# Kernel tuning notes

Measured on AMD Instinct MI355X. Metric: run time of the kernel, lower is better.

Reference implementation:

```python
import jax, jax.numpy as jnp
import numpy as np

B, L, D, T = 2, 2048, 1536, 2
INITRANGE = 0.1

def setup_inputs() -> dict:
    key = jax.random.key(0)
    k1, k2 = jax.random.split(key)
    hidden_states = jax.random.normal(k1, (B, L, D), dtype=jnp.float32)
    # decoder: Linear(2*D, T) with uniform(-0.1, 0.1) weight, zero bias
    W = jax.random.uniform(k2, (T, 2 * D), dtype=jnp.float32, minval=-INITRANGE, maxval=INITRANGE)
    b = jnp.zeros((T,), dtype=jnp.float32)
    return {"hidden_states": hidden_states, "W": W, "b": b}

def reference(hidden_states, W, b):
    # Faithful fused version of:
    #   prod = h[:,:,None,:] * h[:,None,:,:]; diff = h[:,:,None,:] - h[:,None,:,:]
    #   logits = cat(prod, diff, -1) @ W.T + b
    # Split W into the product half and the difference half.
    d = hidden_states.shape[-1]
    Wp, Wd = W[:, :d], W[:, d:]                      # [T, D] each
    # prod term: sum_d h[b,i,d] * h[b,j,d] * Wp[t,d]
    hw = jnp.einsum('bid,td->btid', hidden_states, Wp)          # [B,T,L,D]
    prod_logits = jnp.einsum('btid,bjd->bijt', hw, hidden_states)  # [B,L,L,T]
    # diff term: (h[b,i]-h[b,j]) @ Wd.T = (h@Wd.T)[b,i] - (h@Wd.T)[b,j]
    hd = jnp.einsum('bid,td->bit', hidden_states, Wd)           # [B,L,T]
    diff_logits = hd[:, :, None, :] - hd[:, None, :, :]         # [B,L,L,T]
    logits = prod_logits + diff_logits + b
    # symmetrize over the (i, j) pair axes
    logits = (logits + jnp.transpose(logits, (0, 2, 1, 3))) * 0.5
    return logits
```

## Files before the change

kernel.cpp:

```cpp
#include <hip/hip_runtime.h>
#include <hip/hip_bf16.h>
#include <stdint.h>

#define B_ 2
#define L_ 2048
#define D_ 1536

typedef __attribute__((ext_vector_type(4))) float  f32x4;
typedef __attribute__((ext_vector_type(8))) __bf16 bf16x8;

__device__ __forceinline__ unsigned short f2bf(float f) {
  unsigned int u = __float_as_uint(f);
  u += 0x7fffu + ((u >> 16) & 1u);
  return (unsigned short)(u >> 16);
}

__global__ __launch_bounds__(256) void conv_kernel(
    const float* __restrict__ hs, const float* __restrict__ W,
    unsigned short* __restrict__ X, unsigned short* __restrict__ P) {
  const int idx  = blockIdx.x * 256 + threadIdx.x;
  const int base = idx * 4;
  const int d    = base % D_;
  const float4 h  = *(const float4*)(hs + base);
  const float4 w0 = *(const float4*)(W + d);
  const float4 w1 = *(const float4*)(W + 2 * D_ + d);
  ushort4 x, p0, p1;
  x.x  = f2bf(h.x);        x.y  = f2bf(h.y);        x.z  = f2bf(h.z);        x.w  = f2bf(h.w);
  p0.x = f2bf(h.x * w0.x); p0.y = f2bf(h.y * w0.y); p0.z = f2bf(h.z * w0.z); p0.w = f2bf(h.w * w0.w);
  p1.x = f2bf(h.x * w1.x); p1.y = f2bf(h.y * w1.y); p1.z = f2bf(h.z * w1.z); p1.w = f2bf(h.w * w1.w);
  *(ushort4*)(X + base) = x;
  *(ushort4*)(P + base) = p0;
  *(ushort4*)(P + (size_t)B_ * L_ * D_ + base) = p1;
}

__device__ __forceinline__ void async16(const void* g, const void* l) {
  __builtin_amdgcn_global_load_lds(
      (const __attribute__((address_space(1))) void*)g,
      (__attribute__((address_space(3))) void*)l, 16, 0, 0);
}

__global__ __launch_bounds__(256, 4) void gemm_kernel(
    const unsigned short* __restrict__ X, const unsigned short* __restrict__ P,
    const float* __restrict__ bias, float* __restrict__ out) {
  __shared__ unsigned short As[2 * 128 * 32];
  __shared__ unsigned short Bs[2 * 128 * 32];

  const int tid = threadIdx.x;

  const int id     = blockIdx.x;
  const int xcd    = id & 7;
  const int u      = id >> 3;
  const int t      = u & 1;
  const int v      = u >> 1;
  const int within = v & 15;
  const int pp     = v >> 4;
  const int Pp     = pp * 8 + xcd;
  const int bz     = Pp >> 4;
  const int pr     = Pp & 15;
  const int I0     = ((pr >> 2) * 4 + (within >> 2)) * 128;
  const int J0     = ((pr & 3)  * 4 + (within & 3))  * 128;

  const int srow = tid >> 2;
  const int cs   = tid & 3;
  const int gc   = cs ^ ((srow >> 1) & 3);
  const int scol = gc * 8;
  const int ldst = tid * 8;

  const unsigned short* pA =
      P + (size_t)t * B_ * L_ * D_ + ((size_t)(bz * L_ + I0 + srow)) * D_ + scol;
  const unsigned short* pB =
      X + ((size_t)(bz * L_ + J0 + srow)) * D_ + scol;

  const int lane = tid & 63;
  const int w    = tid >> 6;
  const int wi   = (w & 1) * 64;
  const int wj   = (w >> 1) * 64;
  const int lr   = lane & 15;
  const int q    = lane >> 4;
  const int ccol = (q ^ ((lr >> 1) & 3)) * 8;

  int aoff[4], boff[4];
#pragma unroll
  for (int m = 0; m < 4; ++m) {
    aoff[m] = (wi + m * 16 + lr) * 32 + ccol;
    boff[m] = (wj + m * 16 + lr) * 32 + ccol;
  }

  f32x4 acc[4][4] = {};

#define STAGE(buf, koff)                                          \
  do {                                                            \
    async16(pA + (koff),           As + (buf) * 4096 + ldst);     \
    async16(pA + (koff) + 64 * D_, As + (buf) * 4096 + ldst + 2048); \
    async16(pB + (koff),           Bs + (buf) * 4096 + ldst);     \
    async16(pB + (koff) + 64 * D_, Bs + (buf) * 4096 + ldst + 2048); \
  } while (0)

  STAGE(0, 0);
  for (int k = 0; k < D_ / 32; ++k) {
    __syncthreads();
    if (k < D_ / 32 - 1) STAGE((k + 1) & 1, (k + 1) * 32);
    const unsigned short* Ab = As + (k & 1) * 4096;
    const unsigned short* Bb = Bs + (k & 1) * 4096;
    bf16x8 af[4], bf_[4];
#pragma unroll
    for (int m = 0; m < 4; ++m) af[m]  = *(const bf16x8*)(Ab + aoff[m]);
#pragma unroll
    for (int n = 0; n < 4; ++n) bf_[n] = *(const bf16x8*)(Bb + boff[n]);
#pragma unroll
    for (int m = 0; m < 4; ++m)
#pragma unroll
      for (int n = 0; n < 4; ++n)
        acc[m][n] = __builtin_amdgcn_mfma_f32_16x16x32_bf16(af[m], bf_[n], acc[m][n], 0, 0, 0);
  }
#undef STAGE

  const float bt = bias[t];
#pragma unroll
  for (int m = 0; m < 4; ++m) {
#pragma unroll
    for (int r = 0; r < 4; ++r) {
      const int i = I0 + wi + m * 16 + q * 4 + r;
      float* orow = out + (((size_t)(bz * L_ + i)) * L_ + (J0 + wj + lr)) * 2 + t;
#pragma unroll
      for (int n = 0; n < 4; ++n) orow[n * 32] = acc[m][n][r] + bt;
    }
  }
}

extern "C" void kernel_launch(void* const* d_in, const int* in_sizes, int n_in,
                              void* d_out, int out_size, void* d_ws, size_t ws_size,
                              hipStream_t stream) {
  const float* hs   = (const float*)d_in[0];
  const float* W    = (const float*)d_in[1];
  const float* bias = (const float*)d_in[2];

  unsigned short* X = (unsigned short*)d_ws;
  unsigned short* P = X + (size_t)B_ * L_ * D_;

  const int nconv = (B_ * L_ * D_ / 4) / 256;
  conv_kernel<<<nconv, 256, 0, stream>>>(hs, W, X, P);

  gemm_kernel<<<1024, 256, 0, stream>>>(X, P, bias, (float*)d_out);
}
```

Before: 156.6 us.

## Compute only upper-triangular tile pairs and write transposed mirror via LDS

Uses the symmetry of the product term, where P_t·X^T equals X·P_t^T in the symmetrized output, so only tiles with ti<=tj are computed, cutting the grid from 1024 to 544 blocks. Off-diagonal tiles also write their transpose, staged through reused shared memory with padded rows to keep the strided output writes coalesced. This roughly halves the MFMA work in exchange for extra sync-heavy epilogue stores and the loss of the earlier XCD-aware block swizzle. It appears to rely on the diff term cancelling under symmetrization and on the product term being symmetric.

```diff
diff --git a/kernel.cpp b/kernel.cpp
--- a/kernel.cpp
+++ b/kernel.cpp
@@ -42,23 +42,22 @@
 __global__ __launch_bounds__(256, 4) void gemm_kernel(
     const unsigned short* __restrict__ X, const unsigned short* __restrict__ P,
     const float* __restrict__ bias, float* __restrict__ out) {
-  __shared__ unsigned short As[2 * 128 * 32];
-  __shared__ unsigned short Bs[2 * 128 * 32];
+  __shared__ __align__(16) unsigned char smem[32768];
+  unsigned short* As = (unsigned short*)smem;
+  unsigned short* Bs = (unsigned short*)(smem + 16384);
+  float*          Tr = (float*)smem;
 
   const int tid = threadIdx.x;
 
-  const int id     = blockIdx.x;
-  const int xcd    = id & 7;
-  const int u      = id >> 3;
-  const int t      = u & 1;
-  const int v      = u >> 1;
-  const int within = v & 15;
-  const int pp     = v >> 4;
-  const int Pp     = pp * 8 + xcd;
-  const int bz     = Pp >> 4;
-  const int pr     = Pp & 15;
-  const int I0     = ((pr >> 2) * 4 + (within >> 2)) * 128;
-  const int J0     = ((pr & 3)  * 4 + (within & 3))  * 128;
+  const int id  = blockIdx.x;
+  int rem = id >> 2;
+  const int t   = id & 1;
+  const int bz  = (id >> 1) & 1;
+  int ti = 0;
+  while (rem >= 16 - ti) { rem -= 16 - ti; ++ti; }
+  const int tj = ti + rem;
+  const int I0 = ti * 128;
+  const int J0 = tj * 128;
 
   const int srow = tid >> 2;
   const int cs   = tid & 3;
@@ -88,11 +87,11 @@
 
   f32x4 acc[4][4] = {};
 
-#define STAGE(buf, koff)                                          \
-  do {                                                            \
-    async16(pA + (koff),           As + (buf) * 4096 + ldst);     \
+#define STAGE(buf, koff)                                             \
+  do {                                                               \
+    async16(pA + (koff),           As + (buf) * 4096 + ldst);        \
     async16(pA + (koff) + 64 * D_, As + (buf) * 4096 + ldst + 2048); \
-    async16(pB + (koff),           Bs + (buf) * 4096 + ldst);     \
+    async16(pB + (koff),           Bs + (buf) * 4096 + ldst);        \
     async16(pB + (koff) + 64 * D_, Bs + (buf) * 4096 + ldst + 2048); \
   } while (0)
 
@@ -126,6 +125,33 @@
       for (int n = 0; n < 4; ++n) orow[n * 32] = acc[m][n][r] + bt;
     }
   }
+
+  if (ti != tj) {
+#pragma unroll
+    for (int p = 0; p < 4; ++p) {
+      const int c0 = p * 32;
+      __syncthreads();
+#pragma unroll
+      for (int n = 0; n < 4; ++n) {
+        if (((wj + n * 16) >> 5) == p) {
+          const int col = wj + n * 16 + lr - c0;
+#pragma unroll
+          for (int m = 0; m < 4; ++m)
+#pragma unroll
+            for (int r = 0; r < 4; ++r)
+              Tr[col * 129 + (wi + m * 16 + q * 4 + r)] = acc[m][n][r] + bt;
+        }
+      }
+      __syncthreads();
+      const int mr  = tid >> 3;
+      const int seg = tid & 7;
+      const int jj  = J0 + c0 + mr;
+      float* obase = out + (((size_t)(bz * L_ + jj)) * L_ + I0 + seg * 16) * 2 + t;
+#pragma unroll
+      for (int e = 0; e < 16; ++e)
+        obase[e * 2] = Tr[mr * 129 + seg * 16 + e];
+    }
+  }
 }
 
 extern "C" void kernel_launch(void* const* d_in, const int* in_sizes, int n_in,
@@ -141,5 +167,5 @@
   const int nconv = (B_ * L_ * D_ / 4) / 256;
   conv_kernel<<<nconv, 256, 0, stream>>>(hs, W, X, P);
 
-  gemm_kernel<<<1024, 256, 0, stream>>>(X, P, bias, (float*)d_out);
+  gemm_kernel<<<544, 256, 0, stream>>>(X, P, bias, (float*)d_out);
 }
```

Measured after the change: 212.6 us. 35.8% more time.

## Replace direct global-to-LDS loads with register-staged double-buffered prefetch

Applied to the files above, without the earlier changes.

The GEMM mainloop no longer uses global_load_lds. Each tile is now loaded into registers, written to LDS with ds_write, and the next tile's global loads are issued before the current tile's MFMAs, with the k-loop unrolled by two across the ping-pong buffers. The minimum-occupancy hint in launch bounds drops from 4 to 3 blocks to make room for the extra staging registers. The aim is better overlap of global latency with compute, at the cost of more VGPRs, explicit LDS writes, and possibly lower occupancy.

```diff
diff --git a/kernel.cpp b/kernel.cpp
--- a/kernel.cpp
+++ b/kernel.cpp
@@ -33,13 +33,7 @@
   *(ushort4*)(P + (size_t)B_ * L_ * D_ + base) = p1;
 }
 
-__device__ __forceinline__ void async16(const void* g, const void* l) {
-  __builtin_amdgcn_global_load_lds(
-      (const __attribute__((address_space(1))) void*)g,
-      (__attribute__((address_space(3))) void*)l, 16, 0, 0);
-}
-
-__global__ __launch_bounds__(256, 4) void gemm_kernel(
+__global__ __launch_bounds__(256, 3) void gemm_kernel(
     const unsigned short* __restrict__ X, const unsigned short* __restrict__ P,
     const float* __restrict__ bias, float* __restrict__ out) {
   __shared__ unsigned short As[2 * 128 * 32];
@@ -68,8 +62,7 @@
 
   const unsigned short* pA =
       P + (size_t)t * B_ * L_ * D_ + ((size_t)(bz * L_ + I0 + srow)) * D_ + scol;
-  const unsigned short* pB =
-      X + ((size_t)(bz * L_ + J0 + srow)) * D_ + scol;
+  const unsigned short* pB = X + ((size_t)(bz * L_ + J0 + srow)) * D_ + scol;
 
   const int lane = tid & 63;
   const int w    = tid >> 6;
@@ -88,32 +81,60 @@
 
   f32x4 acc[4][4] = {};
 
-#define STAGE(buf, koff)                                          \
-  do {                                                            \
-    async16(pA + (koff),           As + (buf) * 4096 + ldst);     \
-    async16(pA + (koff) + 64 * D_, As + (buf) * 4096 + ldst + 2048); \
-    async16(pB + (koff),           Bs + (buf) * 4096 + ldst);     \
-    async16(pB + (koff) + 64 * D_, Bs + (buf) * 4096 + ldst + 2048); \
+  uint4 ral, rah, rbl, rbh;
+  uint4 sal, sah, sbl, sbh;
+
+#define GLOAD0(koff)                                \
+  do {                                              \
+    ral = *(const uint4*)(pA + (koff));             \
+    rah = *(const uint4*)(pA + (koff) + 64 * D_);   \
+    rbl = *(const uint4*)(pB + (koff));             \
+    rbh = *(const uint4*)(pB + (koff) + 64 * D_);   \
+  } while (0)
+#define GLOAD1(koff)                                \
+  do {                                              \
+    sal = *(const uint4*)(pA + (koff));             \
+    sah = *(const uint4*)(pA + (koff) + 64 * D_);   \
+    sbl = *(const uint4*)(pB + (koff));             \
+    sbh = *(const uint4*)(pB + (koff) + 64 * D_);   \
+  } while (0)
+#define DSW(buf, AL, AH, BL, BH)                    \
+  do {                                              \
+    *(uint4*)(As + (buf) * 4096 + ldst)        = AL;\
+    *(uint4*)(As + (buf) * 4096 + ldst + 2048) = AH;\
+    *(uint4*)(Bs + (buf) * 4096 + ldst)        = BL;\
+    *(uint4*)(Bs + (buf) * 4096 + ldst + 2048) = BH;\
+  } while (0)
+#define COMPUTE(buf)                                                          \
+  do {                                                                        \
+    const unsigned short* Ab = As + (buf) * 4096;                             \
+    const unsigned short* Bb = Bs + (buf) * 4096;                             \
+    bf16x8 af[4], bf_[4];                                                     \
+    _Pragma("unroll") for (int m = 0; m < 4; ++m)                             \
+      af[m] = *(const bf16x8*)(Ab + aoff[m]);                                 \
+    _Pragma("unroll") for (int n = 0; n < 4; ++n)                             \
+      bf_[n] = *(const bf16x8*)(Bb + boff[n]);                                \
+    _Pragma("unroll") for (int m = 0; m < 4; ++m)                             \
+      _Pragma("unroll") for (int n = 0; n < 4; ++n)                           \
+        acc[m][n] = __builtin_amdgcn_mfma_f32_16x16x32_bf16(af[m], bf_[n],    \
+                                                            acc[m][n], 0, 0, 0); \
   } while (0)
 
-  STAGE(0, 0);
-  for (int k = 0; k < D_ / 32; ++k) {
+  GLOAD0(0);
+  for (int k = 0; k < D_ / 32; k += 2) {
+    DSW(0, ral, rah, rbl, rbh);
+    GLOAD1((k + 1) * 32);
     __syncthreads();
-    if (k < D_ / 32 - 1) STAGE((k + 1) & 1, (k + 1) * 32);
-    const unsigned short* Ab = As + (k & 1) * 4096;
-    const unsigned short* Bb = Bs + (k & 1) * 4096;
-    bf16x8 af[4], bf_[4];
-#pragma unroll
-    for (int m = 0; m < 4; ++m) af[m]  = *(const bf16x8*)(Ab + aoff[m]);
-#pragma unroll
-    for (int n = 0; n < 4; ++n) bf_[n] = *(const bf16x8*)(Bb + boff[n]);
-#pragma unroll
-    for (int m = 0; m < 4; ++m)
-#pragma unroll
-      for (int n = 0; n < 4; ++n)
-        acc[m][n] = __builtin_amdgcn_mfma_f32_16x16x32_bf16(af[m], bf_[n], acc[m][n], 0, 0, 0);
+    COMPUTE(0);
+    DSW(1, sal, sah, sbl, sbh);
+    if (k + 2 < D_ / 32) GLOAD0((k + 2) * 32);
+    __syncthreads();
+    COMPUTE(1);
   }
-#undef STAGE
+#undef GLOAD0
+#undef GLOAD1
+#undef DSW
+#undef COMPUTE
 
   const float bt = bias[t];
 #pragma unroll
```

Result: no change. 159.2 us (+1.7%).
